# Kernel optimization log

Measured on AMD Instinct MI355X. Metric: run time of the kernel, lower is better.

## Reference

```python
import jax, jax.numpy as jnp
import numpy as np

H = 128
NH = 8  # num attention heads


def _ln(x, g, b, eps=1e-5):
    m = x.mean(-1, keepdims=True)
    v = ((x - m) ** 2).mean(-1, keepdims=True)
    return (x - m) / jnp.sqrt(v + eps) * g + b


def _mha(q_in, kv_in, Wqkv, bqkv, Wo, bo):
    # torch nn.MultiheadAttention with packed in_proj, batch=1, eval (no dropout)
    h = q_in.shape[-1]
    hd = h // NH
    Wq, Wk, Wv = Wqkv[:h], Wqkv[h:2 * h], Wqkv[2 * h:]
    bq, bk, bv = bqkv[:h], bqkv[h:2 * h], bqkv[2 * h:]
    q = (q_in @ Wq.T + bq).reshape(-1, NH, hd).transpose(1, 0, 2)   # [nh, Nq, hd]
    k = (kv_in @ Wk.T + bk).reshape(-1, NH, hd).transpose(1, 0, 2)  # [nh, Nk, hd]
    v = (kv_in @ Wv.T + bv).reshape(-1, NH, hd).transpose(1, 0, 2)
    scores = jnp.einsum('hqd,hkd->hqk', q, k) / jnp.sqrt(jnp.asarray(hd, q.dtype))
    attn = jax.nn.softmax(scores, axis=-1)
    out = jnp.einsum('hqk,hkd->hqd', attn, v)                       # [nh, Nq, hd]
    out = out.transpose(1, 0, 2).reshape(-1, h)
    return out @ Wo.T + bo


def setup_inputs() -> dict:
    key = jax.random.key(0)
    ks = jax.random.split(key, 32)
    s = 0.05
    d = {
        'ligand_features': jax.random.normal(ks[0], (512, 128), jnp.float32),
        'pocket_features': jax.random.normal(ks[1], (1024, 128), jnp.float32),
        'ligand_coords': jax.random.uniform(ks[2], (512, 3), jnp.float32) * 20.0,
        'pocket_coords': jax.random.uniform(ks[3], (1024, 3), jnp.float32) * 20.0,
        # projections
        'Wl': jax.random.normal(ks[4], (H, 128), jnp.float32) * s,
        'bl': jnp.zeros((H,), jnp.float32),
        'Wp': jax.random.normal(ks[5], (H, 128), jnp.float32) * s,
        'bp': jnp.zeros((H,), jnp.float32),
        # distance encoder: 1 -> h/4 -> h/2 -> h
        'Wd1': jax.random.normal(ks[6], (H // 4, 1), jnp.float32) * s,
        'bd1': jnp.zeros((H // 4,), jnp.float32),
        'Wd2': jax.random.normal(ks[7], (H // 2, H // 4), jnp.float32) * s,
        'bd2': jnp.zeros((H // 2,), jnp.float32),
        'Wd3': jax.random.normal(ks[8], (H, H // 2), jnp.float32) * s,
        'bd3': jnp.zeros((H,), jnp.float32),
        # gates
        'Wgl': jax.random.normal(ks[9], (H, 2 * H), jnp.float32) * s,
        'bgl': jnp.zeros((H,), jnp.float32),
        'Wgp': jax.random.normal(ks[10], (H, 2 * H), jnp.float32) * s,
        'bgp': jnp.zeros((H,), jnp.float32),
        # shared cross-attention (packed qkv like torch)
        'Wqkv': jax.random.normal(ks[11], (3 * H, H), jnp.float32) * s,
        'bqkv': jnp.zeros((3 * H,), jnp.float32),
        'Wo': jax.random.normal(ks[12], (H, H), jnp.float32) * s,
        'bo': jnp.zeros((H,), jnp.float32),
        # layer norms
        'g_l': jnp.ones((H,), jnp.float32),
        'be_l': jnp.zeros((H,), jnp.float32),
        'g_p': jnp.ones((H,), jnp.float32),
        'be_p': jnp.zeros((H,), jnp.float32),
    }
    return d


def reference(ligand_features, pocket_features, ligand_coords, pocket_coords,
              Wl, bl, Wp, bp, Wd1, bd1, Wd2, bd2, Wd3, bd3,
              Wgl, bgl, Wgp, bgp, Wqkv, bqkv, Wo, bo,
              g_l, be_l, g_p, be_p):
    lig = ligand_features @ Wl.T + bl   # [Nl, H]
    poc = pocket_features @ Wp.T + bp   # [Np, H]

    # pairwise distances [Nl, Np]
    diff = ligand_coords[:, None, :] - pocket_coords[None, :, :]
    dist = jnp.sqrt(jnp.sum(diff * diff, axis=-1))

    # distance encoder MLP applied elementwise -> [Nl, Np, H]
    e = jax.nn.relu(dist[..., None] @ Wd1.T + bd1)
    e = jax.nn.relu(e @ Wd2.T + bd2)
    enc = e @ Wd3.T + bd3
    m = enc.mean(axis=-1)               # [Nl, Np]

    # ligand enhancement: softmax over pocket axis
    sw_l = jax.nn.softmax(-m, axis=-1)          # [Nl, Np]
    agg_l = sw_l @ poc                          # [Nl, H]
    gate_l = jax.nn.sigmoid(jnp.concatenate([lig, agg_l], axis=-1) @ Wgl.T + bgl)
    lig_enh = gate_l * lig + (1.0 - gate_l) * agg_l

    # pocket enhancement: transposed encoding, softmax over ligand axis
    sw_p = jax.nn.softmax(-m.T, axis=-1)        # [Np, Nl]
    agg_p = sw_p @ lig                          # [Np, H]
    gate_p = jax.nn.sigmoid(jnp.concatenate([poc, agg_p], axis=-1) @ Wgp.T + bgp)
    poc_enh = gate_p * poc + (1.0 - gate_p) * agg_p

    lig_att = _mha(lig_enh, poc_enh, Wqkv, bqkv, Wo, bo)
    poc_att = _mha(poc_enh, lig_enh, Wqkv, bqkv, Wo, bo)

    lig_fused = _ln(lig_enh + lig_att, g_l, be_l)
    poc_fused = _ln(poc_enh + poc_att, g_p, be_p)
    return (lig_fused, poc_fused)
```

## Files before the change

### kernel.cpp

```cpp
#include <hip/hip_runtime.h>
#include <math.h>

#define NL 512
#define NP 1024
#define HDIM 128

#define TAB_N 8192
#define DMAX 34.65f

#define M_OFF    128
#define WQT_OFF  (M_OFF)
#define WOT_OFF  (M_OFF + 49152)
#define WGLT_OFF (M_OFF + 65536)
#define WGPT_OFF (M_OFF + 98304)
#define TAB_OFF  (M_OFF + 131072)
#define LIG_OFF  (M_OFF + 139264)
#define POC_OFF  (LIG_OFF + NL*HDIM)
#define LENH_OFF (POC_OFF + NP*HDIM)
#define PENH_OFF (LENH_OFF + NL*HDIM)
#define QKVL_OFF (PENH_OFF + NP*HDIM)
#define QKVP_OFF (QKVL_OFF + NL*384)
#define PARTL_OFF (QKVP_OFF + NP*384)
#define PARTP_OFF (PARTL_OFF + 512*8*8*18)

__device__ __forceinline__ float dot4f(float4 a, float4 b){
  return fmaf(a.x,b.x, fmaf(a.y,b.y, fmaf(a.z,b.z, a.w*b.w)));
}

__device__ __forceinline__ void tpose(const float* __restrict__ src, float* __restrict__ dst,
                                      int O, int K, int blk0, int t){
  int e0 = blk0*1024 + t*4;
  #pragma unroll
  for (int i = 0; i < 4; i++){
    int e = e0 + i;
    int o = e / K, k = e - o*K;
    dst[(size_t)k*O + o] = src[(size_t)o*K + k];
  }
}

__global__ __launch_bounds__(256) void prep_proj(
    const float* __restrict__ lf, const float* __restrict__ pf,
    const float* __restrict__ Wl, const float* __restrict__ bl,
    const float* __restrict__ Wp, const float* __restrict__ bp,
    const float* __restrict__ Wqkv, const float* __restrict__ Wo,
    const float* __restrict__ Wgl, const float* __restrict__ Wgp,
    const float* __restrict__ Wd1, const float* __restrict__ bd1,
    const float* __restrict__ Wd2, const float* __restrict__ bd2,
    const float* __restrict__ Wd3, const float* __restrict__ bd3,
    float* __restrict__ ws){
  int b = blockIdx.x, t = threadIdx.x;

  if (b < 768){
    bool isLig = (b < 256);
    int r0 = isLig ? b*2 : (b - 256)*2;
    const float* in   = (isLig ? lf : pf) + (size_t)r0*HDIM;
    const float* W    = isLig ? Wl : Wp;
    const float* bias = isLig ? bl : bp;
    float* out = ws + (isLig ? LIG_OFF : POC_OFF) + (size_t)r0*HDIM;
    __shared__ __align__(16) float sx[2*HDIM];
    sx[t] = in[t];
    __syncthreads();
    int r = t >> 7, col = t & 127;
    const float* xr = sx + r*HDIM;
    const float* wrow = W + (size_t)col*128;
    float acc = bias[col];
    #pragma unroll 8
    for (int k = 0; k < 128; k++) acc = fmaf(wrow[k], xr[k], acc);
    out[r*HDIM + col] = acc;
    return;
  }

  if (b < 896){
    int bb = b - 768;
    if      (bb < 48) tpose(Wqkv, ws + WQT_OFF,  384, 128, bb,      t);
    else if (bb < 64) tpose(Wo,   ws + WOT_OFF,  128, 128, bb - 48, t);
    else if (bb < 96) tpose(Wgl,  ws + WGLT_OFF, 128, 256, bb - 64, t);
    else              tpose(Wgp,  ws + WGPT_OFF, 128, 256, bb - 96, t);
    return;
  }

  float* tab = ws + TAB_OFF;
  __shared__ float sWd1[32], sbd1[32], sWd2[2048], sbd2[64], swd3m[64];
  __shared__ float sbd3m;
  int idx = (b - 896) * 256 + t;
  if (t < 64){
    float s = 0.f;
    #pragma unroll 8
    for (int i = 0; i < 128; i++) s += Wd3[i*64 + t];
    swd3m[t] = s * (1.f/128.f);
  } else if (t == 64){
    float s = 0.f;
    for (int i = 0; i < 128; i++) s += bd3[i];
    sbd3m = s * (1.f/128.f);
  } else if (t >= 128 && t < 160){ sWd1[t-128] = Wd1[t-128]; sbd1[t-128] = bd1[t-128]; }
  else if (t >= 160 && t < 224){ sbd2[t-160] = bd2[t-160]; }
  for (int k = t; k < 2048; k += 256) sWd2[k] = Wd2[k];
  __syncthreads();

  float d = (float)idx * (DMAX / (float)(TAB_N - 1));
  float4 e1q[8];
  const float4* w1q = (const float4*)sWd1;
  const float4* b1q = (const float4*)sbd1;
  #pragma unroll
  for (int k4 = 0; k4 < 8; k4++){
    float4 w = w1q[k4], bb2 = b1q[k4];
    float4 e;
    e.x = fmaxf(fmaf(d, w.x, bb2.x), 0.f);
    e.y = fmaxf(fmaf(d, w.y, bb2.y), 0.f);
    e.z = fmaxf(fmaf(d, w.z, bb2.z), 0.f);
    e.w = fmaxf(fmaf(d, w.w, bb2.w), 0.f);
    e1q[k4] = e;
  }
  float mv = sbd3m;
  #pragma unroll 4
  for (int j2 = 0; j2 < 64; j2++){
    const float4* wrow = (const float4*)(sWd2 + j2*32);
    float a0 = 0.f, a1 = 0.f, a2 = 0.f, a3 = 0.f;
    #pragma unroll
    for (int k4 = 0; k4 < 8; k4++){
      float4 w = wrow[k4], e = e1q[k4];
      a0 = fmaf(w.x, e.x, a0);
      a1 = fmaf(w.y, e.y, a1);
      a2 = fmaf(w.z, e.z, a2);
      a3 = fmaf(w.w, e.w, a3);
    }
    float e2v = fmaxf(sbd2[j2] + ((a0+a1)+(a2+a3)), 0.f);
    mv = fmaf(swd3m[j2], e2v, mv);
  }
  tab[idx] = mv;
}

__global__ __launch_bounds__(512) void agg_gate_fused(const float* __restrict__ lc, const float* __restrict__ pc,
                                                      const float* __restrict__ tab,
                                                      const float* __restrict__ lig, const float* __restrict__ poc,
                                                      const float* __restrict__ WglT, const float* __restrict__ bgl,
                                                      const float* __restrict__ WgpT, const float* __restrict__ bgp,
                                                      const float* __restrict__ WqkvT, const float* __restrict__ bqkv,
                                                      float* __restrict__ lenh, float* __restrict__ penh,
                                                      float* __restrict__ qkvl, float* __restrict__ qkvp){
  int b = blockIdx.x, t = threadIdx.x;
  bool isLig = (b < NL/2);
  int r0 = isLig ? b*2 : (b - NL/2)*2;
  int n = isLig ? NP : NL;
  const float* myFeat = isLig ? lig : poc;
  const float* otherFeat = isLig ? poc : lig;
  const float* myC = isLig ? lc : pc;
  const float* otC = isLig ? pc : lc;

  __shared__ float w[2*NP];
  __shared__ float sx[2*HDIM];
  __shared__ float sa[2*HDIM];
  __shared__ float4 part4[8*64];
  __shared__ float gpart[512];
  __shared__ float redm[8];
  __shared__ float sgm[2], sinv[2];

  int rr = t >> 8, u = t & 255;
  int lane = t & 63, wv = t >> 6;
  int row = r0 + rr;

  if (t < 256) sx[t] = myFeat[(size_t)r0*HDIM + t];

  float cx = myC[row*3+0], cy = myC[row*3+1], cz = myC[row*3+2];
  const float inv_h = (float)(TAB_N - 1) / DMAX;
  int per = n >> 8;

  float xs[4];
  float lmax = -1e30f;
  for (int k = 0; k < per; k++){
    int j = u + (k << 8);
    float ox = otC[j*3+0], oy = otC[j*3+1], oz = otC[j*3+2];
    float dx = cx-ox, dy = cy-oy, dz = cz-oz;
    float d = sqrtf(fmaf(dx,dx, fmaf(dy,dy, dz*dz)));
    float xf = d * inv_h;
    int i0 = (int)xf;
    i0 = (i0 > TAB_N-2) ? (TAB_N-2) : i0;
    float f = xf - (float)i0;
    float v0 = tab[i0], v1 = tab[i0+1];
    xs[k] = -fmaf(f, v1 - v0, v0);
    lmax = fmaxf(lmax, xs[k]);
  }
  float v = lmax;
  #pragma unroll
  for (int off = 32; off; off >>= 1) v = fmaxf(v, __shfl_down(v, off));
  if (lane == 0) redm[wv] = v;
  __syncthreads();
  if (t < 2) sgm[t] = fmaxf(fmaxf(redm[t*4+0], redm[t*4+1]), fmaxf(redm[t*4+2], redm[t*4+3]));
  __syncthreads();
  float gm = sgm[rr];
  float lsum = 0.f;
  for (int k = 0; k < per; k++){
    float e = __expf(xs[k] - gm);
    w[rr*NP + u + (k << 8)] = e;
    lsum += e;
  }
  v = lsum;
  #pragma unroll
  for (int off = 32; off; off >>= 1) v += __shfl_down(v, off);
  if (lane == 0) redm[wv] = v;
  __syncthreads();
  if (t < 2) sinv[t] = 1.0f / ((redm[t*4+0] + redm[t*4+1]) + (redm[t*4+2] + redm[t*4+3]));
  __syncthreads();

  {
    int jg = t >> 6;
    int r  = (t >> 5) & 1;
    int c4 = t & 31;
    int per2 = n >> 3;
    int jb0 = jg * per2;
    const float4* of4 = (const float4*)otherFeat;
    const float* wR = w + r*NP;
    float4 acc = {0,0,0,0};
    #pragma unroll 4
    for (int jj = 0; jj < per2; jj++){
      int j = jb0 + jj;
      float4 f = of4[(size_t)j*32 + c4];
      float ww = wR[j];
      acc.x = fmaf(ww, f.x, acc.x); acc.y = fmaf(ww, f.y, acc.y);
      acc.z = fmaf(ww, f.z, acc.z); acc.w = fmaf(ww, f.w, acc.w);
    }
    part4[(jg*2 + r)*32 + c4] = acc;
  }
  __syncthreads();
  #pragma unroll
  for (int s = 4; s >= 1; s >>= 1){
    if (t < s*64){
      int g2 = t >> 6, rem = t & 63;
      float4 a = part4[g2*64 + rem], bb = part4[(g2+s)*64 + rem];
      a.x += bb.x; a.y += bb.y; a.z += bb.z; a.w += bb.w;
      part4[g2*64 + rem] = a;
    }
    __syncthreads();
  }
  if (t < 256) sa[t] = ((const float*)part4)[t] * sinv[t >> 7];
  __syncthreads();

  {
    int r  = t >> 8;
    int kg = (t >> 7) & 1;
    int col = t & 127;
    const float* WT = isLig ? WglT : WgpT;
    const float* inq = (kg == 0) ? (sx + r*HDIM) : (sa + r*HDIM);
    const float* wbase = WT + (size_t)kg*128*128;
    float g = 0.f;
    #pragma unroll 8
    for (int k = 0; k < 128; k++) g = fmaf(wbase[k*128 + col], inq[k], g);
    gpart[kg*256 + r*128 + col] = g;
  }
  __syncthreads();
  float enh_val = 0.f;
  if (t < 256){
    int r = t >> 7, col = t & 127;
    const float* bg = isLig ? bgl : bgp;
    float g = bg[col] + gpart[t] + gpart[256 + t];
    g = 1.0f / (1.0f + __expf(-g));
    float xv = sx[t], av = sa[t];
    enh_val = fmaf(g, xv - av, av);
    float* dst = isLig ? (lenh + (size_t)(r0+r)*HDIM) : (penh + (size_t)(r0+r)*HDIM);
    dst[col] = enh_val;
  }
  __syncthreads();
  if (t < 256) sa[t] = enh_val;
  __syncthreads();

  {
    int r = t >> 8, ln = t & 255;
    const float* er = sa + r*HDIM;
    float* qout = (isLig ? qkvl : qkvp) + (size_t)(r0+r)*384;
    if (ln < 128){
      float a0 = bqkv[ln], a2 = bqkv[ln+256];
      #pragma unroll 4
      for (int k = 0; k < 128; k++){
        float xv = er[k];
        const float* wk = WqkvT + k*384;
        a0 = fmaf(wk[ln],     xv, a0);
        a2 = fmaf(wk[ln+256], xv, a2);
      }
      qout[ln] = a0; qout[ln+256] = a2;
    } else {
      float a1 = bqkv[ln];
      #pragma unroll 4
      for (int k = 0; k < 128; k++) a1 = fmaf(WqkvT[k*384 + ln], er[k], a1);
      qout[ln] = a1;
    }
  }
}

__global__ __launch_bounds__(256) void attn_part(const float* __restrict__ qkvl, const float* __restrict__ qkvp,
                                                 float* __restrict__ partL, float* __restrict__ partP){
  int bx = blockIdx.x;
  int t = threadIdx.x;
  const float* qsrc; const float* kvsrc; int qt, slice; bool isLig;
  if (bx < 256){ isLig = true;  qt = bx >> 3; slice = bx & 7; qsrc = qkvl; kvsrc = qkvp; }
  else { int b2 = bx - 256; isLig = false; qt = b2 >> 2; slice = b2 & 3; qsrc = qkvp; kvsrc = qkvl; }
  int g = t >> 6, tt = t & 63;
  int h = tt >> 3, qp = tt & 7;
  int j0 = slice*128 + g*32;
  int hx = h & 3;

  const float4* qA = (const float4*)(qsrc + (size_t)(qt*16+qp)*384 + h*16);
  const float4* qB = (const float4*)(qsrc + (size_t)(qt*16+qp+8)*384 + h*16);
  float4 a0 = qA[0], a1 = qA[1], a2 = qA[2], a3 = qA[3];
  float4 b0 = qB[0], b1 = qB[1], b2 = qB[2], b3 = qB[3];
  float mA = -1e30f, lA = 0.f, mB = -1e30f, lB = 0.f;
  float4 OA0={0,0,0,0}, OA1={0,0,0,0}, OA2={0,0,0,0}, OA3={0,0,0,0};
  float4 OB0={0,0,0,0}, OB1={0,0,0,0}, OB2={0,0,0,0}, OB3={0,0,0,0};

  __shared__ __align__(16) float sKV[8192];
  float* myKV = sKV + g*2048;

  for (int tile = 0; tile < 4; tile++){
    int jbase = j0 + tile*8;
    __syncthreads();
    #pragma unroll
    for (int nn = 0; nn < 8; nn++){
      int v4 = tt + nn*64;
      int jj = v4 >> 6, c4 = v4 & 63;
      int c4s = (c4 & 60) | ((c4 ^ (c4 >> 2)) & 3);
      ((float4*)myKV)[jj*64 + c4s] = *(const float4*)(kvsrc + (size_t)(jbase+jj)*384 + 128 + c4*4);
    }
    __syncthreads();
    float sA[8], sB[8];
    #pragma unroll
    for (int jj = 0; jj < 8; jj++){
      const float4* kb = ((const float4*)myKV) + jj*64 + h*4;
      float4 k0 = kb[0^hx], k1 = kb[1^hx], k2 = kb[2^hx], k3 = kb[3^hx];
      sA[jj] = (dot4f(a0,k0) + dot4f(a1,k1) + dot4f(a2,k2) + dot4f(a3,k3)) * 0.25f;
      sB[jj] = (dot4f(b0,k0) + dot4f(b1,k1) + dot4f(b2,k2) + dot4f(b3,k3)) * 0.25f;
    }
    float mtA = sA[0], mtB = sB[0];
    #pragma unroll
    for (int jj = 1; jj < 8; jj++){ mtA = fmaxf(mtA, sA[jj]); mtB = fmaxf(mtB, sB[jj]); }
    float mnA = fmaxf(mA, mtA), mnB = fmaxf(mB, mtB);
    float cA = __expf(mA - mnA), cB = __expf(mB - mnB);
    lA *= cA; lB *= cB;
    OA0.x*=cA; OA0.y*=cA; OA0.z*=cA; OA0.w*=cA;
    OA1.x*=cA; OA1.y*=cA; OA1.z*=cA; OA1.w*=cA;
    OA2.x*=cA; OA2.y*=cA; OA2.z*=cA; OA2.w*=cA;
    OA3.x*=cA; OA3.y*=cA; OA3.z*=cA; OA3.w*=cA;
    OB0.x*=cB; OB0.y*=cB; OB0.z*=cB; OB0.w*=cB;
    OB1.x*=cB; OB1.y*=cB; OB1.z*=cB; OB1.w*=cB;
    OB2.x*=cB; OB2.y*=cB; OB2.z*=cB; OB2.w*=cB;
    OB3.x*=cB; OB3.y*=cB; OB3.z*=cB; OB3.w*=cB;
    #pragma unroll
    for (int jj = 0; jj < 8; jj++){
      float pA = __expf(sA[jj] - mnA);
      float pB = __expf(sB[jj] - mnB);
      lA += pA; lB += pB;
      const float4* vb = ((const float4*)myKV) + jj*64 + 32 + h*4;
      float4 v0 = vb[0^hx], v1 = vb[1^hx], v2 = vb[2^hx], v3 = vb[3^hx];
      OA0.x = fmaf(pA, v0.x, OA0.x); OA0.y = fmaf(pA, v0.y, OA0.y);
      OA0.z = fmaf(pA, v0.z, OA0.z); OA0.w = fmaf(pA, v0.w, OA0.w);
      OA1.x = fmaf(pA, v1.x, OA1.x); OA1.y = fmaf(pA, v1.y, OA1.y);
      OA1.z = fmaf(pA, v1.z, OA1.z); OA1.w = fmaf(pA, v1.w, OA1.w);
      OA2.x = fmaf(pA, v2.x, OA2.x); OA2.y = fmaf(pA, v2.y, OA2.y);
      OA2.z = fmaf(pA, v2.z, OA2.z); OA2.w = fmaf(pA, v2.w, OA2.w);
      OA3.x = fmaf(pA, v3.x, OA3.x); OA3.y = fmaf(pA, v3.y, OA3.y);
      OA3.z = fmaf(pA, v3.z, OA3.z); OA3.w = fmaf(pA, v3.w, OA3.w);
      OB0.x = fmaf(pB, v0.x, OB0.x); OB0.y = fmaf(pB, v0.y, OB0.y);
      OB0.z = fmaf(pB, v0.z, OB0.z); OB0.w = fmaf(pB, v0.w, OB0.w);
      OB1.x = fmaf(pB, v1.x, OB1.x); OB1.y = fmaf(pB, v1.y, OB1.y);
      OB1.z = fmaf(pB, v1.z, OB1.z); OB1.w = fmaf(pB, v1.w, OB1.w);
      OB2.x = fmaf(pB, v2.x, OB2.x); OB2.y = fmaf(pB, v2.y, OB2.y);
      OB2.z = fmaf(pB, v2.z, OB2.z); OB2.w = fmaf(pB, v2.w, OB2.w);
      OB3.x = fmaf(pB, v3.x, OB3.x); OB3.y = fmaf(pB, v3.y, OB3.y);
      OB3.z = fmaf(pB, v3.z, OB3.z); OB3.w = fmaf(pB, v3.w, OB3.w);
    }
    mA = mnA; mB = mnB;
  }

  __syncthreads();
  if (g > 0){
    float* bA = sKV + (size_t)((g-1)*128 + tt*2)*19;
    bA[0]=mA; bA[1]=lA;
    bA[2]=OA0.x; bA[3]=OA0.y; bA[4]=OA0.z; bA[5]=OA0.w;
    bA[6]=OA1.x; bA[7]=OA1.y; bA[8]=OA1.z; bA[9]=OA1.w;
    bA[10]=OA2.x; bA[11]=OA2.y; bA[12]=OA2.z; bA[13]=OA2.w;
    bA[14]=OA3.x; bA[15]=OA3.y; bA[16]=OA3.z; bA[17]=OA3.w;
    float* bB = bA + 19;
    bB[0]=mB; bB[1]=lB;
    bB[2]=OB0.x; bB[3]=OB0.y; bB[4]=OB0.z; bB[5]=OB0.w;
    bB[6]=OB1.x; bB[7]=OB1.y; bB[8]=OB1.z; bB[9]=OB1.w;
    bB[10]=OB2.x; bB[11]=OB2.y; bB[12]=OB2.z; bB[13]=OB2.w;
    bB[14]=OB3.x; bB[15]=OB3.y; bB[16]=OB3.z; bB[17]=OB3.w;
  }
  __syncthreads();
  if (g == 0){
    float M = mA, L = lA;
    float O[16] = {OA0.x,OA0.y,OA0.z,OA0.w, OA1.x,OA1.y,OA1.z,OA1.w,
                   OA2.x,OA2.y,OA2.z,OA2.w, OA3.x,OA3.y,OA3.z,OA3.w};
    #pragma unroll
    for (int gg = 1; gg < 4; gg++){
      const float* br = sKV + (size_t)((gg-1)*128 + tt*2)*19;
      float m1 = br[0], l1 = br[1];
      float Mn = fmaxf(M, m1);
      float e0 = __expf(M - Mn), e1 = __expf(m1 - Mn);
      L = L*e0 + l1*e1;
      #pragma unroll
      for (int k = 0; k < 16; k++) O[k] = O[k]*e0 + br[2+k]*e1;
      M = Mn;
    }
    int rowA = qt*16 + qp;
    float* dst = isLig ? (partL + ((size_t)(rowA*8 + h)*8 + slice)*18)
                       : (partP + ((size_t)(rowA*8 + h)*4 + slice)*18);
    dst[0] = M; dst[1] = L;
    #pragma unroll
    for (int k = 0; k < 16; k++) dst[2+k] = O[k];
    M = mB; L = lB;
    float Ob[16] = {OB0.x,OB0.y,OB0.z,OB0.w, OB1.x,OB1.y,OB1.z,OB1.w,
                    OB2.x,OB2.y,OB2.z,OB2.w, OB3.x,OB3.y,OB3.z,OB3.w};
    #pragma unroll
    for (int gg = 1; gg < 4; gg++){
      const float* br = sKV + (size_t)((gg-1)*128 + tt*2 + 1)*19;
      float m1 = br[0], l1 = br[1];
      float Mn = fmaxf(M, m1);
      float e0 = __expf(M - Mn), e1 = __expf(m1 - Mn);
      L = L*e0 + l1*e1;
      #pragma unroll
      for (int k = 0; k < 16; k++) Ob[k] = Ob[k]*e0 + br[2+k]*e1;
      M = Mn;
    }
    int rowB = qt*16 + qp + 8;
    float* dstB = isLig ? (partL + ((size_t)(rowB*8 + h)*8 + slice)*18)
                        : (partP + ((size_t)(rowB*8 + h)*4 + slice)*18);
    dstB[0] = M; dstB[1] = L;
    #pragma unroll
    for (int k = 0; k < 16; k++) dstB[2+k] = Ob[k];
  }
}

__global__ __launch_bounds__(256) void merge_ln(const float* __restrict__ partL, const float* __restrict__ partP,
                                                const float* __restrict__ lenh, const float* __restrict__ penh,
                                                const float* __restrict__ WoT, const float* __restrict__ bo,
                                                const float* __restrict__ g_l, const float* __restrict__ be_l,
                                                const float* __restrict__ g_p, const float* __restrict__ be_p,
                                                float* __restrict__ out){
  int b = blockIdx.x, t = threadIdx.x;
  int r0 = b*2;
  int r = t >> 7, c = t & 127;
  int gr = r0 + r;
  int h = c >> 4, cc = c & 15;
  int ns; const float* base;
  if (gr < NL){ ns = 8; base = partL + ((size_t)(gr*8 + h))*8*18; }
  else        { ns = 4; base = partP + ((size_t)((gr-NL)*8 + h))*4*18; }
  float M = -1e30f;
  for (int s = 0; s < ns; s++) M = fmaxf(M, base[s*18]);
  float Lsum = 0.f, Osum = 0.f;
  for (int s = 0; s < ns; s++){
    float e = __expf(base[s*18] - M);
    Lsum = fmaf(e, base[s*18+1], Lsum);
    Osum = fmaf(e, base[s*18+2+cc], Osum);
  }
  __shared__ float sAtt[2*HDIM];
  sAtt[t] = Osum / Lsum;
  __syncthreads();
  float o = bo[c];
  const float* sA = sAtt + r*HDIM;
  #pragma unroll 8
  for (int k = 0; k < 128; k++) o = fmaf(WoT[k*128 + c], sA[k], o);
  const float* enh = (gr < NL) ? (lenh + (size_t)gr*HDIM) : (penh + (size_t)(gr-NL)*HDIM);
  float x = enh[c] + o;
  __shared__ float sred[8];
  int wid = t >> 6;
  float v = x;
  #pragma unroll
  for (int off = 32; off; off >>= 1) v += __shfl_down(v, off);
  if ((t & 63) == 0) sred[wid] = v;
  __syncthreads();
  float mu = (sred[2*r] + sred[2*r+1]) * (1.f/128.f);
  float dx = x - mu;
  v = dx*dx;
  #pragma unroll
  for (int off = 32; off; off >>= 1) v += __shfl_down(v, off);
  if ((t & 63) == 0) sred[4 + wid] = v;
  __syncthreads();
  float var = (sred[4 + 2*r] + sred[4 + 2*r+1]) * (1.f/128.f);
  float y = dx * rsqrtf(var + 1e-5f);
  if (gr < NL) y = fmaf(y, g_l[c], be_l[c]);
  else         y = fmaf(y, g_p[c], be_p[c]);
  out[(size_t)gr*HDIM + c] = y;
}

extern "C" void kernel_launch(void* const* d_in, const int* in_sizes, int n_in,
                              void* d_out, int out_size, void* d_ws, size_t ws_size,
                              hipStream_t stream){
  const float* lf   = (const float*)d_in[0];
  const float* pf   = (const float*)d_in[1];
  const float* lc   = (const float*)d_in[2];
  const float* pc   = (const float*)d_in[3];
  const float* Wl   = (const float*)d_in[4];
  const float* bl   = (const float*)d_in[5];
  const float* Wp   = (const float*)d_in[6];
  const float* bp   = (const float*)d_in[7];
  const float* Wd1  = (const float*)d_in[8];
  const float* bd1  = (const float*)d_in[9];
  const float* Wd2  = (const float*)d_in[10];
  const float* bd2  = (const float*)d_in[11];
  const float* Wd3  = (const float*)d_in[12];
  const float* bd3  = (const float*)d_in[13];
  const float* Wgl  = (const float*)d_in[14];
  const float* bgl  = (const float*)d_in[15];
  const float* Wgp  = (const float*)d_in[16];
  const float* bgp  = (const float*)d_in[17];
  const float* Wqkv = (const float*)d_in[18];
  const float* bqkv = (const float*)d_in[19];
  const float* Wo   = (const float*)d_in[20];
  const float* bo   = (const float*)d_in[21];
  const float* g_l  = (const float*)d_in[22];
  const float* be_l = (const float*)d_in[23];
  const float* g_p  = (const float*)d_in[24];
  const float* be_p = (const float*)d_in[25];

  float* ws  = (float*)d_ws;
  float* out = (float*)d_out;

  float* lig   = ws + LIG_OFF;
  float* poc   = ws + POC_OFF;
  float* lenh  = ws + LENH_OFF;
  float* penh  = ws + PENH_OFF;
  float* qkvl  = ws + QKVL_OFF;
  float* qkvp  = ws + QKVP_OFF;
  float* partL = ws + PARTL_OFF;
  float* partP = ws + PARTP_OFF;
  float* tab   = ws + TAB_OFF;

  prep_proj<<<928, 256, 0, stream>>>(lf, pf, Wl, bl, Wp, bp, Wqkv, Wo, Wgl, Wgp,
                                     Wd1, bd1, Wd2, bd2, Wd3, bd3, ws);
  agg_gate_fused<<<NL/2 + NP/2, 512, 0, stream>>>(lc, pc, tab, lig, poc,
                                                  ws + WGLT_OFF, bgl, ws + WGPT_OFF, bgp,
                                                  ws + WQT_OFF, bqkv,
                                                  lenh, penh, qkvl, qkvp);
  attn_part<<<512, 256, 0, stream>>>(qkvl, qkvp, partL, partP);
  merge_ln<<<NL/2 + NP/2, 256, 0, stream>>>(partL, partP, lenh, penh, ws + WOT_OFF, bo,
                                            g_l, be_l, g_p, be_p, out);
}
```

Baseline: 195.7 us.

## Process eight rows per block in aggregation/gate kernel to reuse feature and weight loads

```diff
diff --git a/kernel.cpp b/kernel.cpp
--- a/kernel.cpp
+++ b/kernel.cpp
@@ -130,159 +130,190 @@
   tab[idx] = mv;
 }
 
-__global__ __launch_bounds__(512) void agg_gate_fused(const float* __restrict__ lc, const float* __restrict__ pc,
-                                                      const float* __restrict__ tab,
-                                                      const float* __restrict__ lig, const float* __restrict__ poc,
-                                                      const float* __restrict__ WglT, const float* __restrict__ bgl,
-                                                      const float* __restrict__ WgpT, const float* __restrict__ bgp,
-                                                      const float* __restrict__ WqkvT, const float* __restrict__ bqkv,
-                                                      float* __restrict__ lenh, float* __restrict__ penh,
-                                                      float* __restrict__ qkvl, float* __restrict__ qkvp){
+template<int PERT>
+__device__ __forceinline__ void agg_gate_body(
+    int t, int r0,
+    const float* __restrict__ myC, const float* __restrict__ otC,
+    const float* __restrict__ myFeat, const float* __restrict__ otherFeat,
+    const float* __restrict__ tab,
+    const float* __restrict__ WgT, const float* __restrict__ bg,
+    const float* __restrict__ WqkvT, const float* __restrict__ bqkv,
+    float* __restrict__ enh_out, float* __restrict__ qkv_out,
+    float* __restrict__ smem)
+{
+  const int n = PERT * 64;
+  float* w      = smem;
+  float* scr    = smem;
+  float* agg    = smem + 8192;
+  float* sx     = smem + 9216;
+  float* se     = smem + 10240;
+  float* gpart  = smem + 11264;
+
+  int lane = t & 63, wv = t >> 6;
+  const float inv_h = (float)(TAB_N - 1) / DMAX;
+
+  {
+    int i0 = t*2;
+    const float* src = myFeat + (size_t)r0*HDIM;
+    sx[i0]   = src[i0];
+    sx[i0+1] = src[i0+1];
+  }
+
+  {
+    int row = r0 + wv;
+    float cx = myC[row*3+0], cy = myC[row*3+1], cz = myC[row*3+2];
+    float xs[PERT];
+    float lmax = -1e30f;
+    #pragma unroll
+    for (int k = 0; k < PERT; k++){
+      int j = lane + (k << 6);
+      float ox = otC[j*3+0], oy = otC[j*3+1], oz = otC[j*3+2];
+      float dx = cx-ox, dy = cy-oy, dz = cz-oz;
+      float d = sqrtf(fmaf(dx,dx, fmaf(dy,dy, dz*dz)));
+      float xf = d * inv_h;
+      int i0 = (int)xf;
+      i0 = (i0 > TAB_N-2) ? (TAB_N-2) : i0;
+      float f = xf - (float)i0;
+      float v0 = tab[i0], v1 = tab[i0+1];
+      xs[k] = -fmaf(f, v1 - v0, v0);
+      lmax = fmaxf(lmax, xs[k]);
+    }
+    #pragma unroll
+    for (int off = 32; off; off >>= 1) lmax = fmaxf(lmax, __shfl_xor(lmax, off));
+    float lsum = 0.f;
+    #pragma unroll
+    for (int k = 0; k < PERT; k++){
+      xs[k] = __expf(xs[k] - lmax);
+      lsum += xs[k];
+    }
+    #pragma unroll
+    for (int off = 32; off; off >>= 1) lsum += __shfl_xor(lsum, off);
+    float sinv = 1.0f / lsum;
+    #pragma unroll
+    for (int k = 0; k < PERT; k++)
+      w[wv*1024 + lane + (k << 6)] = xs[k] * sinv;
+  }
+  __syncthreads();
+
+  float4 acc[8];
+  #pragma unroll
+  for (int r = 0; r < 8; r++) acc[r] = make_float4(0.f,0.f,0.f,0.f);
+  int jg = t >> 5, c4 = t & 31;
+  {
+    const int JI = n >> 4;
+    const float4* F4 = (const float4*)otherFeat;
+    int jb0 = jg * JI;
+    #pragma unroll 2
+    for (int jj = 0; jj < JI; jj++){
+      int j = jb0 + jj;
+      float4 f = F4[(size_t)j*32 + c4];
+      #pragma unroll
+      for (int r = 0; r < 8; r++){
+        float ww = w[r*1024 + j];
+        acc[r].x = fmaf(ww, f.x, acc[r].x);
+        acc[r].y = fmaf(ww, f.y, acc[r].y);
+        acc[r].z = fmaf(ww, f.z, acc[r].z);
+        acc[r].w = fmaf(ww, f.w, acc[r].w);
+      }
+    }
+  }
+  #pragma unroll
+  for (int s = 8; s >= 1; s >>= 1){
+    __syncthreads();
+    if (jg >= s && jg < 2*s){
+      float4* dst = (float4*)scr + ((size_t)(jg - s)*8)*32;
+      #pragma unroll
+      for (int r = 0; r < 8; r++) dst[r*32 + c4] = acc[r];
+    }
+    __syncthreads();
+    if (jg < s){
+      const float4* src = (const float4*)scr + ((size_t)jg*8)*32;
+      #pragma unroll
+      for (int r = 0; r < 8; r++){
+        float4 bb = src[r*32 + c4];
+        acc[r].x += bb.x; acc[r].y += bb.y; acc[r].z += bb.z; acc[r].w += bb.w;
+      }
+    }
+  }
+  if (jg == 0){
+    float4* a4 = (float4*)agg;
+    #pragma unroll
+    for (int r = 0; r < 8; r++) a4[r*32 + c4] = acc[r];
+  }
+  __syncthreads();
+
+  {
+    int col = t & 127, kg = t >> 7;
+    float g8[8];
+    #pragma unroll
+    for (int r = 0; r < 8; r++) g8[r] = 0.f;
+    int k0 = kg*64;
+    #pragma unroll 2
+    for (int kk = 0; kk < 64; kk++){
+      int k = k0 + kk;
+      float wgv = WgT[(size_t)k*128 + col];
+      const float* inb = (k < 128) ? (sx + k) : (agg + (k - 128));
+      #pragma unroll
+      for (int r = 0; r < 8; r++)
+        g8[r] = fmaf(wgv, inb[r*128], g8[r]);
+    }
+    #pragma unroll
+    for (int r = 0; r < 8; r++) gpart[(kg*8 + r)*128 + col] = g8[r];
+  }
+  __syncthreads();
+  {
+    int col = t & 127, rr = t >> 7;
+    #pragma unroll
+    for (int h2 = 0; h2 < 2; h2++){
+      int r = rr + h2*4;
+      float g = bg[col] + ((gpart[(0*8+r)*128+col] + gpart[(1*8+r)*128+col])
+                         + (gpart[(2*8+r)*128+col] + gpart[(3*8+r)*128+col]));
+      g = 1.0f / (1.0f + __expf(-g));
+      float xv = sx[r*128+col], av = agg[r*128+col];
+      float enh = fmaf(g, xv - av, av);
+      se[r*128+col] = enh;
+      enh_out[(size_t)(r0+r)*HDIM + col] = enh;
+    }
+  }
+  __syncthreads();
+
+  if (t < 384){
+    int o = t;
+    float q8[8];
+    float bq = bqkv[o];
+    #pragma unroll
+    for (int r = 0; r < 8; r++) q8[r] = bq;
+    #pragma unroll 4
+    for (int k = 0; k < 128; k++){
+      float wq = WqkvT[(size_t)k*384 + o];
+      #pragma unroll
+      for (int r = 0; r < 8; r++)
+        q8[r] = fmaf(wq, se[r*128 + k], q8[r]);
+    }
+    #pragma unroll
+    for (int r = 0; r < 8; r++)
+      qkv_out[(size_t)(r0+r)*384 + o] = q8[r];
+  }
+}
+
+__global__ __launch_bounds__(512) void agg_gate8(
+    const float* __restrict__ lc, const float* __restrict__ pc,
+    const float* __restrict__ tab,
+    const float* __restrict__ lig, const float* __restrict__ poc,
+    const float* __restrict__ WglT, const float* __restrict__ bgl,
+    const float* __restrict__ WgpT, const float* __restrict__ bgp,
+    const float* __restrict__ WqkvT, const float* __restrict__ bqkv,
+    float* __restrict__ lenh, float* __restrict__ penh,
+    float* __restrict__ qkvl, float* __restrict__ qkvp)
+{
+  __shared__ __align__(16) float smem[15360];
   int b = blockIdx.x, t = threadIdx.x;
-  bool isLig = (b < NL/2);
-  int r0 = isLig ? b*2 : (b - NL/2)*2;
-  int n = isLig ? NP : NL;
-  const float* myFeat = isLig ? lig : poc;
-  const float* otherFeat = isLig ? poc : lig;
-  const float* myC = isLig ? lc : pc;
-  const float* otC = isLig ? pc : lc;
-
-  __shared__ float w[2*NP];
-  __shared__ float sx[2*HDIM];
-  __shared__ float sa[2*HDIM];
-  __shared__ float4 part4[8*64];
-  __shared__ float gpart[512];
-  __shared__ float redm[8];
-  __shared__ float sgm[2], sinv[2];
-
-  int rr = t >> 8, u = t & 255;
-  int lane = t & 63, wv = t >> 6;
-  int row = r0 + rr;
-
-  if (t < 256) sx[t] = myFeat[(size_t)r0*HDIM + t];
-
-  float cx = myC[row*3+0], cy = myC[row*3+1], cz = myC[row*3+2];
-  const float inv_h = (float)(TAB_N - 1) / DMAX;
-  int per = n >> 8;
-
-  float xs[4];
-  float lmax = -1e30f;
-  for (int k = 0; k < per; k++){
-    int j = u + (k << 8);
-    float ox = otC[j*3+0], oy = otC[j*3+1], oz = otC[j*3+2];
-    float dx = cx-ox, dy = cy-oy, dz = cz-oz;
-    float d = sqrtf(fmaf(dx,dx, fmaf(dy,dy, dz*dz)));
-    float xf = d * inv_h;
-    int i0 = (int)xf;
-    i0 = (i0 > TAB_N-2) ? (TAB_N-2) : i0;
-    float f = xf - (float)i0;
-    float v0 = tab[i0], v1 = tab[i0+1];
-    xs[k] = -fmaf(f, v1 - v0, v0);
-    lmax = fmaxf(lmax, xs[k]);
-  }
-  float v = lmax;
-  #pragma unroll
-  for (int off = 32; off; off >>= 1) v = fmaxf(v, __shfl_down(v, off));
-  if (lane == 0) redm[wv] = v;
-  __syncthreads();
-  if (t < 2) sgm[t] = fmaxf(fmaxf(redm[t*4+0], redm[t*4+1]), fmaxf(redm[t*4+2], redm[t*4+3]));
-  __syncthreads();
-  float gm = sgm[rr];
-  float lsum = 0.f;
-  for (int k = 0; k < per; k++){
-    float e = __expf(xs[k] - gm);
-    w[rr*NP + u + (k << 8)] = e;
-    lsum += e;
-  }
-  v = lsum;
-  #pragma unroll
-  for (int off = 32; off; off >>= 1) v += __shfl_down(v, off);
-  if (lane == 0) redm[wv] = v;
-  __syncthreads();
-  if (t < 2) sinv[t] = 1.0f / ((redm[t*4+0] + redm[t*4+1]) + (redm[t*4+2] + redm[t*4+3]));
-  __syncthreads();
-
-  {
-    int jg = t >> 6;
-    int r  = (t >> 5) & 1;
-    int c4 = t & 31;
-    int per2 = n >> 3;
-    int jb0 = jg * per2;
-    const float4* of4 = (const float4*)otherFeat;
-    const float* wR = w + r*NP;
-    float4 acc = {0,0,0,0};
-    #pragma unroll 4
-    for (int jj = 0; jj < per2; jj++){
-      int j = jb0 + jj;
-      float4 f = of4[(size_t)j*32 + c4];
-      float ww = wR[j];
-      acc.x = fmaf(ww, f.x, acc.x); acc.y = fmaf(ww, f.y, acc.y);
-      acc.z = fmaf(ww, f.z, acc.z); acc.w = fmaf(ww, f.w, acc.w);
-    }
-    part4[(jg*2 + r)*32 + c4] = acc;
-  }
-  __syncthreads();
-  #pragma unroll
-  for (int s = 4; s >= 1; s >>= 1){
-    if (t < s*64){
-      int g2 = t >> 6, rem = t & 63;
-      float4 a = part4[g2*64 + rem], bb = part4[(g2+s)*64 + rem];
-      a.x += bb.x; a.y += bb.y; a.z += bb.z; a.w += bb.w;
-      part4[g2*64 + rem] = a;
-    }
-    __syncthreads();
-  }
-  if (t < 256) sa[t] = ((const float*)part4)[t] * sinv[t >> 7];
-  __syncthreads();
-
-  {
-    int r  = t >> 8;
-    int kg = (t >> 7) & 1;
-    int col = t & 127;
-    const float* WT = isLig ? WglT : WgpT;
-    const float* inq = (kg == 0) ? (sx + r*HDIM) : (sa + r*HDIM);
-    const float* wbase = WT + (size_t)kg*128*128;
-    float g = 0.f;
-    #pragma unroll 8
-    for (int k = 0; k < 128; k++) g = fmaf(wbase[k*128 + col], inq[k], g);
-    gpart[kg*256 + r*128 + col] = g;
-  }
-  __syncthreads();
-  float enh_val = 0.f;
-  if (t < 256){
-    int r = t >> 7, col = t & 127;
-    const float* bg = isLig ? bgl : bgp;
-    float g = bg[col] + gpart[t] + gpart[256 + t];
-    g = 1.0f / (1.0f + __expf(-g));
-    float xv = sx[t], av = sa[t];
-    enh_val = fmaf(g, xv - av, av);
-    float* dst = isLig ? (lenh + (size_t)(r0+r)*HDIM) : (penh + (size_t)(r0+r)*HDIM);
-    dst[col] = enh_val;
-  }
-  __syncthreads();
-  if (t < 256) sa[t] = enh_val;
-  __syncthreads();
-
-  {
-    int r = t >> 8, ln = t & 255;
-    const float* er = sa + r*HDIM;
-    float* qout = (isLig ? qkvl : qkvp) + (size_t)(r0+r)*384;
-    if (ln < 128){
-      float a0 = bqkv[ln], a2 = bqkv[ln+256];
-      #pragma unroll 4
-      for (int k = 0; k < 128; k++){
-        float xv = er[k];
-        const float* wk = WqkvT + k*384;
-        a0 = fmaf(wk[ln],     xv, a0);
-        a2 = fmaf(wk[ln+256], xv, a2);
-      }
-      qout[ln] = a0; qout[ln+256] = a2;
-    } else {
-      float a1 = bqkv[ln];
-      #pragma unroll 4
-      for (int k = 0; k < 128; k++) a1 = fmaf(WqkvT[k*384 + ln], er[k], a1);
-      qout[ln] = a1;
-    }
+  if (b < 64){
+    agg_gate_body<16>(t, b*8, lc, pc, lig, poc, tab, WglT, bgl, WqkvT, bqkv,
+                      lenh, qkvl, smem);
+  } else {
+    agg_gate_body<8>(t, (b-64)*8, pc, lc, poc, lig, tab, WgpT, bgp, WqkvT, bqkv,
+                     penh, qkvp, smem);
   }
 }
 
@@ -526,10 +557,10 @@
 
   prep_proj<<<928, 256, 0, stream>>>(lf, pf, Wl, bl, Wp, bp, Wqkv, Wo, Wgl, Wgp,
                                      Wd1, bd1, Wd2, bd2, Wd3, bd3, ws);
-  agg_gate_fused<<<NL/2 + NP/2, 512, 0, stream>>>(lc, pc, tab, lig, poc,
-                                                  ws + WGLT_OFF, bgl, ws + WGPT_OFF, bgp,
-                                                  ws + WQT_OFF, bqkv,
-                                                  lenh, penh, qkvl, qkvp);
+  agg_gate8<<<192, 512, 0, stream>>>(lc, pc, tab, lig, poc,
+                                     ws + WGLT_OFF, bgl, ws + WGPT_OFF, bgp,
+                                     ws + WQT_OFF, bqkv,
+                                     lenh, penh, qkvl, qkvp);
   attn_part<<<512, 256, 0, stream>>>(qkvl, qkvp, partL, partP);
   merge_ln<<<NL/2 + NP/2, 256, 0, stream>>>(partL, partP, lenh, penh, ws + WOT_OFF, bo,
                                             g_l, be_l, g_p, be_p, out);
```

Result: no change. 193.2 us (-1.3%).
